# Kernel tuning notes

Hardware: AMD Instinct MI355X
Metric: run time of the kernel (lower is better)

The kernel has to match this reference:

```python
import jax, jax.numpy as jnp
import numpy as np

N = 1024
B = 128
DT = 0.1
STEPS = 10

def setup_inputs() -> dict:
    key = jax.random.key(0)
    k1, k2, k3 = jax.random.split(key, 3)
    theta_init = jax.random.normal(k1, (B, N), dtype=jnp.float32)
    K0 = jax.random.normal(k2, (N, N), dtype=jnp.float32) * 0.1
    K = (K0 + K0.T) / 2  # symmetric coupling matrix, as in __init__
    omega = jax.random.normal(k3, (N,), dtype=jnp.float32) * 0.1
    K_global = jnp.asarray(0.5, dtype=jnp.float32)
    return {"theta_init": theta_init, "K": K, "omega": omega, "K_global": K_global}

def _compute_coherence(theta):
    # Kuramoto order parameter r = |<e^{i theta}>| over oscillator axis
    cos_mean = jnp.cos(theta).mean(axis=-1)
    sin_mean = jnp.sin(theta).mean(axis=-1)
    return jnp.sqrt(cos_mean ** 2 + sin_mean ** 2)

def reference(theta_init, K, omega, K_global):
    n = theta_init.shape[-1]

    def step(theta, _):
        # theta_diff[b, i, j] = theta[b, j] - theta[b, i]
        theta_diff = theta[..., None, :] - theta[..., :, None]  # [B, n, n]
        coupling_sum = (K * jnp.sin(theta_diff)).sum(axis=-1)   # [B, n]
        dtheta = omega + (K_global / n) * coupling_sum
        theta_new = theta + DT * dtheta
        # wrap to (-pi, pi]
        theta_new = jnp.arctan2(jnp.sin(theta_new), jnp.cos(theta_new))
        return theta_new, None

    theta, _ = jax.lax.scan(step, theta_init, None, length=STEPS)
    coherence = _compute_coherence(theta)
    return theta, coherence
```

## Files before the change

### kernel.cpp

```cpp
#include <hip/hip_runtime.h>
#include <math.h>

#define KN 1024
#define KB 128
#define KDT 0.1f
#define KSTEPS 10
#define KMAGIC 0xB0000000u
#define PI_F 3.14159265358979f
#define TWO_PI_F 6.28318530717959f

typedef __attribute__((ext_vector_type(8))) short short8;
typedef __attribute__((ext_vector_type(4))) float floatx4;
typedef unsigned long long u64;

__device__ __forceinline__ unsigned short f2bf(float f) {
    unsigned u = __float_as_uint(f);
    u += 0x7FFF + ((u >> 16) & 1);
    return (unsigned short)(u >> 16);
}

__device__ __forceinline__ unsigned xidx(int grp, int b15, int k) {
    return (unsigned)(grp * 16384 + (k >> 5) * 512 + ((k >> 1) & 3) * 128 +
                      ((k >> 3) & 3) * 32 + b15 * 2 + (k & 1));
}

__global__ __launch_bounds__(512)
void k_main(const float* __restrict__ theta0,
            const float* __restrict__ Kmat,
            const float* __restrict__ omega,
            const float* __restrict__ kg,
            float* __restrict__ out_theta,
            float* __restrict__ out_coh,
            unsigned* __restrict__ flags,
            float* __restrict__ acc,
            unsigned* __restrict__ xA,
            unsigned* __restrict__ xB)
{
    const int grp = blockIdx.x >> 5;
    const int b0  = grp * 16;
    const int i0  = (blockIdx.x & 31) * 32;

    const int tid  = threadIdx.x;
    const int lane = tid & 63;
    const int kq   = tid >> 6;
    const int r16  = lane & 15;
    const int quad = lane >> 4;

    __shared__ float ldsY[8][2][16][34];

    if ((blockIdx.x & 31) == 0 && tid < 16) {
        __hip_atomic_store(&acc[(b0 + tid) * 16], 0.f, __ATOMIC_RELAXED,
                           __HIP_MEMORY_SCOPE_AGENT);
        __hip_atomic_store(&acc[2048 + (b0 + tid) * 16], 0.f, __ATOMIC_RELAXED,
                           __HIP_MEMORY_SCOPE_AGENT);
    }

    short8 bfrag[2][4];
    #pragma unroll
    for (int wi = 0; wi < 2; ++wi) {
        const float* kp = Kmat + (size_t)(i0 + wi * 16 + r16) * KN + kq * 128 + quad * 8;
        #pragma unroll
        for (int it = 0; it < 4; ++it) {
            const float4 v0 = *reinterpret_cast<const float4*>(kp + it * 32);
            const float4 v1 = *reinterpret_cast<const float4*>(kp + it * 32 + 4);
            short8 b_;
            b_[0] = (short)f2bf(v0.x); b_[1] = (short)f2bf(v0.y);
            b_[2] = (short)f2bf(v0.z); b_[3] = (short)f2bf(v0.w);
            b_[4] = (short)f2bf(v1.x); b_[5] = (short)f2bf(v1.y);
            b_[6] = (short)f2bf(v1.z); b_[7] = (short)f2bf(v1.w);
            bfrag[wi][it] = b_;
        }
    }

    const int eb = b0 + (tid >> 5);
    const int ei = i0 + (tid & 31);
    float th_reg = theta0[(size_t)eb * KN + ei];
    const float omg = omega[ei];
    float sn, cs;
    __sincosf(th_reg, &sn, &cs);
    __hip_atomic_store(&xA[xidx(grp, eb & 15, ei)],
                       (unsigned)f2bf(sn) | ((unsigned)f2bf(cs) << 16),
                       __ATOMIC_RELAXED, __HIP_MEMORY_SCOPE_AGENT);
    const float scale = kg[0] * (1.0f / (float)KN);

    __syncthreads();
    if (tid == 0)
        __hip_atomic_store(&flags[blockIdx.x], KMAGIC + 0u,
                           __ATOMIC_RELAXED, __HIP_MEMORY_SCOPE_AGENT);

    auto wait_chunks = [&](unsigned tgt) {
        unsigned polls = 0;
        for (;;) {
            unsigned v = tgt;
            if (lane < 4)
                v = __hip_atomic_load(&flags[grp * 32 + kq * 4 + lane],
                                      __ATOMIC_RELAXED, __HIP_MEMORY_SCOPE_AGENT);
            if (__ballot(v >= tgt) == ~0ull) break;
            if (++polls > 4000000u) break;
            __builtin_amdgcn_s_sleep(2);
        }
    };

    const unsigned* xcur = xA;
    unsigned* xnxt = xB;
    float s2 = sn, c2 = cs;
    for (int s = 0; s < KSTEPS; ++s) {
        wait_chunks(KMAGIC + (unsigned)s);

        const u64* xg = (const u64*)xcur + grp * 8192 + kq * 1024 + lane;
        u64 aw[4][4];
        #pragma unroll
        for (int it = 0; it < 4; ++it)
            #pragma unroll
            for (int jj = 0; jj < 4; ++jj)
                aw[it][jj] = __hip_atomic_load((u64*)(xg + it * 256 + jj * 64),
                                               __ATOMIC_RELAXED,
                                               __HIP_MEMORY_SCOPE_AGENT);
        floatx4 accS[2] = {{0.f,0.f,0.f,0.f},{0.f,0.f,0.f,0.f}};
        floatx4 accC[2] = {{0.f,0.f,0.f,0.f},{0.f,0.f,0.f,0.f}};
        #pragma unroll
        for (int it = 0; it < 4; ++it) {
            short8 a_s, a_c;
            #pragma unroll
            for (int jj = 0; jj < 4; ++jj) {
                unsigned lo = (unsigned)aw[it][jj];
                unsigned hi = (unsigned)(aw[it][jj] >> 32);
                a_s[jj * 2]     = (short)(lo & 0xffffu);
                a_c[jj * 2]     = (short)(lo >> 16);
                a_s[jj * 2 + 1] = (short)(hi & 0xffffu);
                a_c[jj * 2 + 1] = (short)(hi >> 16);
            }
            #pragma unroll
            for (int wi = 0; wi < 2; ++wi) {
                accS[wi] = __builtin_amdgcn_mfma_f32_16x16x32_bf16(a_s, bfrag[wi][it], accS[wi], 0, 0, 0);
                accC[wi] = __builtin_amdgcn_mfma_f32_16x16x32_bf16(a_c, bfrag[wi][it], accC[wi], 0, 0, 0);
            }
        }
        #pragma unroll
        for (int wi = 0; wi < 2; ++wi)
            #pragma unroll
            for (int r = 0; r < 4; ++r) {
                ldsY[kq][0][quad * 4 + r][wi * 16 + r16] = accS[wi][r];
                ldsY[kq][1][quad * 4 + r][wi * 16 + r16] = accC[wi][r];
            }
        __syncthreads();

        {
            const int bl = tid >> 5, ilo = tid & 31;
            float Ys = 0.f, Yc = 0.f;
            #pragma unroll
            for (int q = 0; q < 8; ++q) {
                Ys += ldsY[q][0][bl][ilo];
                Yc += ldsY[q][1][bl][ilo];
            }
            const float coupling = cs * Ys - sn * Yc;
            float tn = th_reg + KDT * (omg + scale * coupling);
            __sincosf(tn, &s2, &c2);
            if (tn > PI_F)       tn -= TWO_PI_F;
            else if (tn < -PI_F) tn += TWO_PI_F;
            th_reg = tn;
            sn = s2; cs = c2;
        }
        if (s < KSTEPS - 1) {
            __hip_atomic_store(&xnxt[xidx(grp, eb & 15, ei)],
                               (unsigned)f2bf(s2) | ((unsigned)f2bf(c2) << 16),
                               __ATOMIC_RELAXED, __HIP_MEMORY_SCOPE_AGENT);
            __syncthreads();
            if (tid == 0)
                __hip_atomic_store(&flags[blockIdx.x], KMAGIC + (unsigned)(s + 1),
                                   __ATOMIC_RELAXED, __HIP_MEMORY_SCOPE_AGENT);
            const unsigned* t = xcur; xcur = xnxt; xnxt = (unsigned*)t;
        } else {
            out_theta[(size_t)eb * KN + ei] = th_reg;
        }
    }

    __syncthreads();
    float* red = &ldsY[0][0][0][0];
    red[tid]       = s2;
    red[512 + tid] = c2;
    __syncthreads();
    if (tid < 16) {
        float ss = 0.f, cc = 0.f;
        #pragma unroll
        for (int il2 = 0; il2 < 32; ++il2) {
            ss += red[tid * 32 + il2];
            cc += red[512 + tid * 32 + il2];
        }
        atomicAdd(&acc[(b0 + tid) * 16], ss);
        atomicAdd(&acc[2048 + (b0 + tid) * 16], cc);
    }
    __syncthreads();
    if (tid == 0)
        __hip_atomic_store(&flags[blockIdx.x], KMAGIC + (unsigned)KSTEPS,
                           __ATOMIC_RELAXED, __HIP_MEMORY_SCOPE_AGENT);

    if ((blockIdx.x & 31) == 0) {
        if (tid < 64) {
            const unsigned tgt = KMAGIC + (unsigned)KSTEPS;
            unsigned polls = 0;
            for (;;) {
                unsigned v = tgt;
                if (lane < 32)
                    v = __hip_atomic_load(&flags[grp * 32 + lane],
                                          __ATOMIC_RELAXED, __HIP_MEMORY_SCOPE_AGENT);
                if (__ballot(v >= tgt) == ~0ull) break;
                if (++polls > 4000000u) break;
                __builtin_amdgcn_s_sleep(2);
            }
        }
        __syncthreads();
        if (tid < 16) {
            float sv = __hip_atomic_load(&acc[(b0 + tid) * 16],
                                         __ATOMIC_RELAXED, __HIP_MEMORY_SCOPE_AGENT);
            float cv = __hip_atomic_load(&acc[2048 + (b0 + tid) * 16],
                                         __ATOMIC_RELAXED, __HIP_MEMORY_SCOPE_AGENT);
            float sm = sv * (1.0f / (float)KN);
            float cm = cv * (1.0f / (float)KN);
            out_coh[b0 + tid] = sqrtf(cm * cm + sm * sm);
        }
    }
}

extern "C" void kernel_launch(void* const* d_in, const int* in_sizes, int n_in,
                              void* d_out, int out_size, void* d_ws, size_t ws_size,
                              hipStream_t stream)
{
    (void)in_sizes; (void)n_in; (void)out_size; (void)ws_size;

    const float* theta0 = (const float*)d_in[0];
    const float* Kmat   = (const float*)d_in[1];
    const float* omega  = (const float*)d_in[2];
    const float* kg     = (const float*)d_in[3];

    float* out_theta = (float*)d_out;
    float* out_coh   = out_theta + (size_t)KB * KN;

    unsigned* flags = (unsigned*)d_ws;
    float* acc      = (float*)((char*)d_ws + 4096);
    unsigned* xA    = (unsigned*)((char*)d_ws + 4096 + 16384);
    unsigned* xB    = xA + (size_t)KB * KN;

    k_main<<<256, 512, 0, stream>>>(theta0, Kmat, omega, kg,
                                    out_theta, out_coh, flags, acc, xA, xB);
}
```

Baseline: 97.46 us.

## Replace block-level step barriers with per-wave flags and triple-buffered exchange

Each wave now publishes its own readiness flag after its store drains, and consumers poll 32 per-wave flags, so the __syncthreads before every flag publish is gone. The exchange buffer is tripled and the LDS reduction buffer doubled, which removes write-after-read hazards once the intra-block barrier no longer orders steps. The initial theta load and flag publish are moved ahead of the K fragment conversion so other blocks can start earlier. The cost is more flag polling traffic per wave, more workspace and LDS, and correctness now rests on the per-wave vmcnt waits and buffer rotation.

```diff
diff --git a/kernel.cpp b/kernel.cpp
--- a/kernel.cpp
+++ b/kernel.cpp
@@ -32,13 +32,14 @@
             float* __restrict__ out_theta,
             float* __restrict__ out_coh,
             unsigned* __restrict__ flags,
+            unsigned* __restrict__ eflags,
             float* __restrict__ acc,
-            unsigned* __restrict__ xA,
-            unsigned* __restrict__ xB)
+            unsigned* __restrict__ xbuf)
 {
     const int grp = blockIdx.x >> 5;
     const int b0  = grp * 16;
-    const int i0  = (blockIdx.x & 31) * 32;
+    const int ib  = blockIdx.x & 31;
+    const int i0  = ib * 32;
 
     const int tid  = threadIdx.x;
     const int lane = tid & 63;
@@ -46,14 +47,33 @@
     const int r16  = lane & 15;
     const int quad = lane >> 4;
 
-    __shared__ float ldsY[8][2][16][34];
-
-    if ((blockIdx.x & 31) == 0 && tid < 16) {
+    __shared__ float ldsY[2][8][2][16][34];
+
+    if (ib == 0 && tid < 16) {
         __hip_atomic_store(&acc[(b0 + tid) * 16], 0.f, __ATOMIC_RELAXED,
                            __HIP_MEMORY_SCOPE_AGENT);
         __hip_atomic_store(&acc[2048 + (b0 + tid) * 16], 0.f, __ATOMIC_RELAXED,
                            __HIP_MEMORY_SCOPE_AGENT);
     }
+
+    const int eb = b0 + (tid >> 5);
+    const int ei = i0 + (tid & 31);
+    float th_reg = theta0[(size_t)eb * KN + ei];
+    const float omg = omega[ei];
+    float sn, cs;
+    __sincosf(th_reg, &sn, &cs);
+    const unsigned xoff = xidx(grp, tid >> 5, ei);
+    unsigned* xb[3] = {xbuf, xbuf + (size_t)KB * KN, xbuf + 2 * (size_t)KB * KN};
+
+    __hip_atomic_store(&xb[0][xoff],
+                       (unsigned)f2bf(sn) | ((unsigned)f2bf(cs) << 16),
+                       __ATOMIC_RELAXED, __HIP_MEMORY_SCOPE_AGENT);
+    const int myflag = grp * 256 + ib * 8 + kq;
+    asm volatile("s_waitcnt vmcnt(0)" ::: "memory");
+    if (lane == 0)
+        __hip_atomic_store(&flags[myflag], KMAGIC + 0u,
+                           __ATOMIC_RELAXED, __HIP_MEMORY_SCOPE_AGENT);
+    const float scale = kg[0] * (1.0f / (float)KN);
 
     short8 bfrag[2][4];
     #pragma unroll
@@ -72,42 +92,25 @@
         }
     }
 
-    const int eb = b0 + (tid >> 5);
-    const int ei = i0 + (tid & 31);
-    float th_reg = theta0[(size_t)eb * KN + ei];
-    const float omg = omega[ei];
-    float sn, cs;
-    __sincosf(th_reg, &sn, &cs);
-    __hip_atomic_store(&xA[xidx(grp, eb & 15, ei)],
-                       (unsigned)f2bf(sn) | ((unsigned)f2bf(cs) << 16),
-                       __ATOMIC_RELAXED, __HIP_MEMORY_SCOPE_AGENT);
-    const float scale = kg[0] * (1.0f / (float)KN);
-
-    __syncthreads();
-    if (tid == 0)
-        __hip_atomic_store(&flags[blockIdx.x], KMAGIC + 0u,
-                           __ATOMIC_RELAXED, __HIP_MEMORY_SCOPE_AGENT);
-
-    auto wait_chunks = [&](unsigned tgt) {
+    auto wait_waves = [&](unsigned tgt) {
         unsigned polls = 0;
         for (;;) {
             unsigned v = tgt;
-            if (lane < 4)
-                v = __hip_atomic_load(&flags[grp * 32 + kq * 4 + lane],
+            if (lane < 32)
+                v = __hip_atomic_load(&flags[grp * 256 + kq * 32 + lane],
                                       __ATOMIC_RELAXED, __HIP_MEMORY_SCOPE_AGENT);
             if (__ballot(v >= tgt) == ~0ull) break;
             if (++polls > 4000000u) break;
             __builtin_amdgcn_s_sleep(2);
         }
+        asm volatile("" ::: "memory");
     };
 
-    const unsigned* xcur = xA;
-    unsigned* xnxt = xB;
     float s2 = sn, c2 = cs;
     for (int s = 0; s < KSTEPS; ++s) {
-        wait_chunks(KMAGIC + (unsigned)s);
-
-        const u64* xg = (const u64*)xcur + grp * 8192 + kq * 1024 + lane;
+        wait_waves(KMAGIC + (unsigned)s);
+
+        const u64* xg = (const u64*)xb[s % 3] + grp * 8192 + kq * 1024 + lane;
         u64 aw[4][4];
         #pragma unroll
         for (int it = 0; it < 4; ++it)
@@ -136,12 +139,13 @@
                 accC[wi] = __builtin_amdgcn_mfma_f32_16x16x32_bf16(a_c, bfrag[wi][it], accC[wi], 0, 0, 0);
             }
         }
+        const int lb = s & 1;
         #pragma unroll
         for (int wi = 0; wi < 2; ++wi)
             #pragma unroll
             for (int r = 0; r < 4; ++r) {
-                ldsY[kq][0][quad * 4 + r][wi * 16 + r16] = accS[wi][r];
-                ldsY[kq][1][quad * 4 + r][wi * 16 + r16] = accC[wi][r];
+                ldsY[lb][kq][0][quad * 4 + r][wi * 16 + r16] = accS[wi][r];
+                ldsY[lb][kq][1][quad * 4 + r][wi * 16 + r16] = accC[wi][r];
             }
         __syncthreads();
 
@@ -150,8 +154,8 @@
             float Ys = 0.f, Yc = 0.f;
             #pragma unroll
             for (int q = 0; q < 8; ++q) {
-                Ys += ldsY[q][0][bl][ilo];
-                Yc += ldsY[q][1][bl][ilo];
+                Ys += ldsY[lb][q][0][bl][ilo];
+                Yc += ldsY[lb][q][1][bl][ilo];
             }
             const float coupling = cs * Ys - sn * Yc;
             float tn = th_reg + KDT * (omg + scale * coupling);
@@ -162,21 +166,20 @@
             sn = s2; cs = c2;
         }
         if (s < KSTEPS - 1) {
-            __hip_atomic_store(&xnxt[xidx(grp, eb & 15, ei)],
+            __hip_atomic_store(&xb[(s + 1) % 3][xoff],
                                (unsigned)f2bf(s2) | ((unsigned)f2bf(c2) << 16),
                                __ATOMIC_RELAXED, __HIP_MEMORY_SCOPE_AGENT);
-            __syncthreads();
-            if (tid == 0)
-                __hip_atomic_store(&flags[blockIdx.x], KMAGIC + (unsigned)(s + 1),
+            asm volatile("s_waitcnt vmcnt(0)" ::: "memory");
+            if (lane == 0)
+                __hip_atomic_store(&flags[myflag], KMAGIC + (unsigned)(s + 1),
                                    __ATOMIC_RELAXED, __HIP_MEMORY_SCOPE_AGENT);
-            const unsigned* t = xcur; xcur = xnxt; xnxt = (unsigned*)t;
         } else {
             out_theta[(size_t)eb * KN + ei] = th_reg;
         }
     }
 
     __syncthreads();
-    float* red = &ldsY[0][0][0][0];
+    float* red = &ldsY[0][0][0][0][0];
     red[tid]       = s2;
     red[512 + tid] = c2;
     __syncthreads();
@@ -192,23 +195,23 @@
     }
     __syncthreads();
     if (tid == 0)
-        __hip_atomic_store(&flags[blockIdx.x], KMAGIC + (unsigned)KSTEPS,
+        __hip_atomic_store(&eflags[blockIdx.x], KMAGIC,
                            __ATOMIC_RELAXED, __HIP_MEMORY_SCOPE_AGENT);
 
-    if ((blockIdx.x & 31) == 0) {
+    if (ib == 0) {
         if (tid < 64) {
-            const unsigned tgt = KMAGIC + (unsigned)KSTEPS;
             unsigned polls = 0;
             for (;;) {
-                unsigned v = tgt;
+                unsigned v = KMAGIC;
                 if (lane < 32)
-                    v = __hip_atomic_load(&flags[grp * 32 + lane],
+                    v = __hip_atomic_load(&eflags[grp * 32 + lane],
                                           __ATOMIC_RELAXED, __HIP_MEMORY_SCOPE_AGENT);
-                if (__ballot(v >= tgt) == ~0ull) break;
+                if (__ballot(v >= KMAGIC) == ~0ull) break;
                 if (++polls > 4000000u) break;
                 __builtin_amdgcn_s_sleep(2);
             }
         }
+        asm volatile("" ::: "memory");
         __syncthreads();
         if (tid < 16) {
             float sv = __hip_atomic_load(&acc[(b0 + tid) * 16],
@@ -236,11 +239,12 @@
     float* out_theta = (float*)d_out;
     float* out_coh   = out_theta + (size_t)KB * KN;
 
-    unsigned* flags = (unsigned*)d_ws;
-    float* acc      = (float*)((char*)d_ws + 4096);
-    unsigned* xA    = (unsigned*)((char*)d_ws + 4096 + 16384);
-    unsigned* xB    = xA + (size_t)KB * KN;
+    unsigned* flags  = (unsigned*)d_ws;
+    unsigned* eflags = (unsigned*)((char*)d_ws + 8192);
+    float* acc       = (float*)((char*)d_ws + 16384);
+    unsigned* xbuf   = (unsigned*)((char*)d_ws + 32768);
 
     k_main<<<256, 512, 0, stream>>>(theta0, Kmat, omega, kg,
-                                    out_theta, out_coh, flags, acc, xA, xB);
-}
+                                    out_theta, out_coh, flags, eflags,
+                                    acc, xbuf);
+}
```

Result: slower. 110.9 us (+13.8%).
